# Performance work log

Hardware: AMD Instinct MI355X
Metric: run time of the kernel (lower is better)

## Reference

```python
import jax, jax.numpy as jnp
import numpy as np

EPS = 1e-06

def feature_map(x):
    # ELU + 1 feature map (default in LinearAttention)
    return jax.nn.elu(x) + 1.0

def setup_inputs() -> dict:
    key = jax.random.key(0)
    kq, kk, kv = jax.random.split(key, 3)
    N, L, H, D = 4, 8192, 16, 64
    queries = jax.random.normal(kq, (N, L, H, D), dtype=jnp.float32)
    keys = jax.random.normal(kk, (N, L, H, D), dtype=jnp.float32)
    values = jax.random.normal(kv, (N, L, H, D), dtype=jnp.float32)
    return {"queries": queries, "keys": keys, "values": values}

def reference(queries, keys, values):
    # Q, K: [N, L, H, D] after ELU+1 feature map
    Q = feature_map(queries)
    K = feature_map(keys)
    # KV state: [N, H, D, M]
    KV = jnp.einsum('nshd,nshm->nhdm', K, values)
    # normalizer: Z[n,l,h] = 1 / (Q . sum_s K + eps)
    Z = 1.0 / (jnp.einsum('nlhd,nhd->nlh', Q, K.sum(axis=1)) + EPS)
    # NOTE: faithful to original: KV (nhdm) is labeled 'nhmd' in the einsum,
    # i.e. KV is used transposed on its last two axes (requires D == M).
    V = jnp.einsum('nlhd,nhmd,nlh->nlhm', Q, KV, Z)
    return V
```

## Files before the change

kernel.cpp:

```cpp
#include <hip/hip_runtime.h>
#include <hip/hip_bf16.h>

#define LDIM 8192
#define HDIM 16
#define DDIM 64
#define NHEADPAIR 64
#define ROWSTRIDE 1024
#define KVSZ 4160
#define EPSF 1e-6f
#define CHUNKS 128
#define RPB 64
#define LROW 36

typedef float f32x4 __attribute__((ext_vector_type(4)));
typedef short s16x8 __attribute__((ext_vector_type(8)));

__device__ __forceinline__ float featmap(float x) {
    return x > 0.0f ? x + 1.0f : __expf(x);
}

__device__ __forceinline__ unsigned int pack_bf16x2(float a, float b) {
    union { __hip_bfloat162 h; unsigned int u; } x;
    x.h = __float22bfloat162_rn(make_float2(a, b));
    return x.u;
}

__device__ __forceinline__ unsigned short bf16_of(float a) {
    union { __hip_bfloat16 h; unsigned short u; } cv;
    cv.h = __float2bfloat16(a);
    return cv.u;
}

__device__ __forceinline__ int swz(int d) { return ((d >> 3) & 3) << 2; }

__global__ __launch_bounds__(256) void kv_oneshot_kernel(
    const float* __restrict__ Kp, const float* __restrict__ Vp,
    unsigned short* __restrict__ part)
{
    __shared__ unsigned int KT[64 * LROW];
    __shared__ unsigned int VT[64 * LROW];

    const int nh   = blockIdx.x;
    const int ch   = blockIdx.y;
    const int n    = nh >> 4;
    const int h    = nh & 15;
    const int t    = threadIdx.x;
    const int wave = t >> 6;
    const int lane = t & 63;

    const bool isK   = (t < 128);
    const int  uw    = (t >> 6) & 1;
    const int  col16 = lane & 15;
    const int  rv    = lane >> 4;
    const float* Sp  = isK ? Kp : Vp;
    const size_t base = (((size_t)n * LDIM + (size_t)ch * RPB) * HDIM + h) * DDIM
                      + col16 * 4;
    unsigned int* T = isK ? KT : VT;

#pragma unroll
    for (int g = 0; g < 4; ++g) {
        const int gg = uw * 4 + g;
        const int r1 = gg * 8 + rv;
        const int r2 = r1 + 4;
        float4 L1 = *(const float4*)(Sp + base + (size_t)r1 * ROWSTRIDE);
        float4 L2 = *(const float4*)(Sp + base + (size_t)r2 * ROWSTRIDE);
        float a[4] = { L1.x, L1.y, L1.z, L1.w };
        float b[4] = { L2.x, L2.y, L2.z, L2.w };
        if (isK) {
#pragma unroll
            for (int j = 0; j < 4; ++j) { a[j] = featmap(a[j]); b[j] = featmap(b[j]); }
        }
        const int slot = gg * 4 + rv;
#pragma unroll
        for (int j = 0; j < 4; ++j) {
            const int d = col16 * 4 + j;
            T[d * LROW + (slot ^ swz(d))] = pack_bf16x2(a[j], b[j]);
        }
    }
    __syncthreads();

    const int fr = lane & 15;
    const int fk = lane >> 4;
    const int d0 = wave * 16;

    f32x4 acc[4];
    f32x4 zac = (f32x4){0.f, 0.f, 0.f, 0.f};
#pragma unroll
    for (int mb = 0; mb < 4; ++mb) acc[mb] = (f32x4){0.f, 0.f, 0.f, 0.f};
    s16x8 ones;
#pragma unroll
    for (int i = 0; i < 8; ++i) ones[i] = (short)0x3F80;

    const int dA = d0 + fr;
#pragma unroll
    for (int kk = 0; kk < 2; ++kk) {
        const int slot = kk * 16 + fk * 4;
        s16x8 A = *(const s16x8*)&KT[dA * LROW + (slot ^ swz(dA))];
        zac = __builtin_amdgcn_mfma_f32_16x16x32_bf16(A, ones, zac, 0, 0, 0);
#pragma unroll
        for (int mb = 0; mb < 4; ++mb) {
            const int m = mb * 16 + fr;
            s16x8 B = *(const s16x8*)&VT[m * LROW + (slot ^ swz(m))];
            acc[mb] = __builtin_amdgcn_mfma_f32_16x16x32_bf16(A, B, acc[mb], 0, 0, 0);
        }
    }

    unsigned short* p = part + ((size_t)nh * CHUNKS + ch) * KVSZ;
#pragma unroll
    for (int mb = 0; mb < 4; ++mb)
#pragma unroll
        for (int reg = 0; reg < 4; ++reg)
            p[(d0 + fk * 4 + reg) * 64 + mb * 16 + fr] = bf16_of(acc[mb][reg]);
    if (fr == 0)
#pragma unroll
        for (int reg = 0; reg < 4; ++reg)
            p[4096 + d0 + fk * 4 + reg] = bf16_of(zac[reg]);
}

__global__ __launch_bounds__(256) void kv_reduce_kernel(
    const unsigned short* __restrict__ part, unsigned short* __restrict__ kvh)
{
    const int nh = blockIdx.y;
    const int e  = blockIdx.x * 256 + threadIdx.x;
    if (e >= KVSZ) return;
    float s = 0.0f;
    for (int c = 0; c < CHUNKS; ++c) {
        union { unsigned short u; __hip_bfloat16 h; } cv;
        cv.u = part[((size_t)nh * CHUNKS + c) * KVSZ + e];
        s += __bfloat162float(cv.h);
    }
    kvh[(size_t)nh * KVSZ + e] = bf16_of(s);
}

__global__ __launch_bounds__(256) void attn_mfma_kernel(
    const float* __restrict__ Qp, const unsigned short* __restrict__ kvh,
    float* __restrict__ out)
{
    __shared__ unsigned int kvU[64][36];
    __shared__ unsigned int ksU[36];
    __shared__ unsigned int qU[128][36];

    const int nh = blockIdx.y;
    const int n  = nh >> 4;
    const int h  = nh & 15;
    const int t  = threadIdx.x;

    {
        const unsigned int* kvg = (const unsigned int*)(kvh + (size_t)nh * KVSZ);
        const int r  = t >> 2;
        const int c0 = (t & 3) * 8;
        uint4 x = *(const uint4*)(kvg + r * 32 + c0);
        uint4 y = *(const uint4*)(kvg + r * 32 + c0 + 4);
        *(uint4*)&kvU[r][c0]     = x;
        *(uint4*)&kvU[r][c0 + 4] = y;
        if (t < 32) ksU[t] = kvg[2048 + t];
    }

    {
        const int qr = t >> 1;
        const float* qg = Qp + ((((size_t)n * LDIM) + (size_t)blockIdx.x * 128 + qr)
                                * HDIM + h) * DDIM + (t & 1) * 32;
        unsigned int q[16];
#pragma unroll
        for (int j = 0; j < 8; ++j) {
            float4 f = *(const float4*)(qg + j * 4);
            q[2 * j]     = pack_bf16x2(featmap(f.x), featmap(f.y));
            q[2 * j + 1] = pack_bf16x2(featmap(f.z), featmap(f.w));
        }
        uint4* dst = (uint4*)&qU[qr][(t & 1) * 16];
        dst[0] = make_uint4(q[0],  q[1],  q[2],  q[3]);
        dst[1] = make_uint4(q[4],  q[5],  q[6],  q[7]);
        dst[2] = make_uint4(q[8],  q[9],  q[10], q[11]);
        dst[3] = make_uint4(q[12], q[13], q[14], q[15]);
    }
    __syncthreads();

    const int wave = t >> 6;
    const int lane = t & 63;
    const int fr = lane & 15;
    const int fk = lane >> 4;

    s16x8 bF[4][2], kF[2];
#pragma unroll
    for (int mt = 0; mt < 4; ++mt)
#pragma unroll
        for (int kk = 0; kk < 2; ++kk)
            bF[mt][kk] = *(const s16x8*)&kvU[mt * 16 + fr][kk * 16 + fk * 4];
#pragma unroll
    for (int kk = 0; kk < 2; ++kk)
        kF[kk] = *(const s16x8*)&ksU[kk * 16 + fk * 4];

    f32x4 acc[2][4];
    f32x4 zac[2];
#pragma unroll
    for (int lt = 0; lt < 2; ++lt) {
        zac[lt] = (f32x4){0.f, 0.f, 0.f, 0.f};
#pragma unroll
        for (int mt = 0; mt < 4; ++mt) acc[lt][mt] = (f32x4){0.f, 0.f, 0.f, 0.f};
    }

#pragma unroll
    for (int kk = 0; kk < 2; ++kk) {
#pragma unroll
        for (int lt = 0; lt < 2; ++lt) {
            s16x8 A = *(const s16x8*)&qU[wave * 32 + lt * 16 + fr][kk * 16 + fk * 4];
            zac[lt] = __builtin_amdgcn_mfma_f32_16x16x32_bf16(A, kF[kk], zac[lt], 0, 0, 0);
#pragma unroll
            for (int mt = 0; mt < 4; ++mt)
                acc[lt][mt] = __builtin_amdgcn_mfma_f32_16x16x32_bf16(
                    A, bF[mt][kk], acc[lt][mt], 0, 0, 0);
        }
    }

#pragma unroll
    for (int lt = 0; lt < 2; ++lt) {
#pragma unroll
        for (int reg = 0; reg < 4; ++reg) {
            const int row = blockIdx.x * 128 + wave * 32 + lt * 16 + fk * 4 + reg;
            const float z = 1.0f / (zac[lt][reg] + EPSF);
            float* orow = out + (((size_t)n * LDIM + row) * HDIM + h) * DDIM;
#pragma unroll
            for (int mt = 0; mt < 4; ++mt)
                orow[mt * 16 + fr] = acc[lt][mt][reg] * z;
        }
    }
}

extern "C" void kernel_launch(void* const* d_in, const int* in_sizes, int n_in,
                              void* d_out, int out_size, void* d_ws, size_t ws_size,
                              hipStream_t stream) {
    const float* Q = (const float*)d_in[0];
    const float* K = (const float*)d_in[1];
    const float* V = (const float*)d_in[2];
    float* out = (float*)d_out;

    unsigned short* part = (unsigned short*)d_ws;
    unsigned short* kvh  = part + (size_t)NHEADPAIR * CHUNKS * KVSZ;

    dim3 g1(NHEADPAIR, CHUNKS);
    kv_oneshot_kernel<<<g1, 256, 0, stream>>>(K, V, part);
    dim3 gr((KVSZ + 255) / 256, NHEADPAIR);
    kv_reduce_kernel<<<gr, 256, 0, stream>>>(part, kvh);
    dim3 g2(LDIM / 128, NHEADPAIR);
    attn_mfma_kernel<<<g2, 256, 0, stream>>>(Q, kvh, out);
}
```

Measured before the change: 156.3 us.

## Restructure KV partial kernel to load 8 heads per block with dense rows

The KV partial kernel now has each 512-thread block cover 8 heads (half the heads of a batch) and 128 rows, looped in four 32-row tiles. Each row segment it loads is then a contiguous 512-byte span across heads, so global reads coalesce better. Halving the chunk count also halves the partial writes and the work of the reduce kernel. The costs are fewer blocks in the grid (8x64), a barrier pair per tile, and padded LDS strides that replace the XOR swizzle.

```diff
diff --git a/kernel.cpp b/kernel.cpp
--- a/kernel.cpp
+++ b/kernel.cpp
@@ -8,9 +8,12 @@
 #define ROWSTRIDE 1024
 #define KVSZ 4160
 #define EPSF 1e-6f
-#define CHUNKS 128
-#define RPB 64
-#define LROW 36
+#define CHUNKS 64
+#define RPB 128
+#define TROWS 32
+#define NT 4
+#define DSTR 17
+#define HSTR (64 * DSTR + 5)
 
 typedef float f32x4 __attribute__((ext_vector_type(4)));
 typedef short s16x8 __attribute__((ext_vector_type(8)));
@@ -31,90 +34,114 @@
     return cv.u;
 }
 
-__device__ __forceinline__ int swz(int d) { return ((d >> 3) & 3) << 2; }
-
-__global__ __launch_bounds__(256) void kv_oneshot_kernel(
+__global__ __launch_bounds__(512) void kv_dense_kernel(
     const float* __restrict__ Kp, const float* __restrict__ Vp,
     unsigned short* __restrict__ part)
 {
-    __shared__ unsigned int KT[64 * LROW];
-    __shared__ unsigned int VT[64 * LROW];
-
-    const int nh   = blockIdx.x;
+    __shared__ unsigned int KT[8 * HSTR];
+    __shared__ unsigned int VT[8 * HSTR];
+
+    const int nhf  = blockIdx.x;
+    const int n    = nhf >> 1;
+    const int half = nhf & 1;
     const int ch   = blockIdx.y;
-    const int n    = nh >> 4;
-    const int h    = nh & 15;
     const int t    = threadIdx.x;
     const int wave = t >> 6;
     const int lane = t & 63;
 
-    const bool isK   = (t < 128);
-    const int  uw    = (t >> 6) & 1;
-    const int  col16 = lane & 15;
-    const int  rv    = lane >> 4;
-    const float* Sp  = isK ? Kp : Vp;
-    const size_t base = (((size_t)n * LDIM + (size_t)ch * RPB) * HDIM + h) * DDIM
-                      + col16 * 4;
-    unsigned int* T = isK ? KT : VT;
-
-#pragma unroll
-    for (int g = 0; g < 4; ++g) {
-        const int gg = uw * 4 + g;
-        const int r1 = gg * 8 + rv;
-        const int r2 = r1 + 4;
-        float4 L1 = *(const float4*)(Sp + base + (size_t)r1 * ROWSTRIDE);
-        float4 L2 = *(const float4*)(Sp + base + (size_t)r2 * ROWSTRIDE);
-        float a[4] = { L1.x, L1.y, L1.z, L1.w };
-        float b[4] = { L2.x, L2.y, L2.z, L2.w };
-        if (isK) {
-#pragma unroll
-            for (int j = 0; j < 4; ++j) { a[j] = featmap(a[j]); b[j] = featmap(b[j]); }
-        }
-        const int slot = gg * 4 + rv;
-#pragma unroll
-        for (int j = 0; j < 4; ++j) {
-            const int d = col16 * 4 + j;
-            T[d * LROW + (slot ^ swz(d))] = pack_bf16x2(a[j], b[j]);
-        }
-    }
-    __syncthreads();
+    const int rb    = t >> 7;
+    const int pos   = t & 127;
+    const int headl = pos >> 4;
+    const int dq    = pos & 15;
+
+    const float4* K4 = (const float4*)Kp;
+    const float4* V4 = (const float4*)Vp;
 
     const int fr = lane & 15;
     const int fk = lane >> 4;
-    const int d0 = wave * 16;
-
-    f32x4 acc[4];
-    f32x4 zac = (f32x4){0.f, 0.f, 0.f, 0.f};
-#pragma unroll
-    for (int mb = 0; mb < 4; ++mb) acc[mb] = (f32x4){0.f, 0.f, 0.f, 0.f};
+
+    f32x4 acc[4][4];
+    f32x4 zac[4];
+#pragma unroll
+    for (int b = 0; b < 4; ++b) {
+        zac[b] = (f32x4){0.f, 0.f, 0.f, 0.f};
+#pragma unroll
+        for (int mb = 0; mb < 4; ++mb) acc[b][mb] = (f32x4){0.f, 0.f, 0.f, 0.f};
+    }
     s16x8 ones;
 #pragma unroll
     for (int i = 0; i < 8; ++i) ones[i] = (short)0x3F80;
 
-    const int dA = d0 + fr;
-#pragma unroll
-    for (int kk = 0; kk < 2; ++kk) {
-        const int slot = kk * 16 + fk * 4;
-        s16x8 A = *(const s16x8*)&KT[dA * LROW + (slot ^ swz(dA))];
-        zac = __builtin_amdgcn_mfma_f32_16x16x32_bf16(A, ones, zac, 0, 0, 0);
+    unsigned int* KTh = &KT[headl * HSTR];
+    unsigned int* VTh = &VT[headl * HSTR];
+    const unsigned int* KTw = &KT[wave * HSTR];
+    const unsigned int* VTw = &VT[wave * HSTR];
+
+    for (int tt = 0; tt < NT; ++tt) {
+        const size_t rowbase = (size_t)n * LDIM + (size_t)ch * RPB + tt * TROWS;
+
+#pragma unroll
+        for (int pb = 0; pb < 4; ++pb) {
+            const int rlo = rb + 8 * pb;
+            const int rhi = rlo + 4;
+            const size_t gl = (rowbase + rlo) * 256 + half * 128 + headl * 16 + dq;
+            const size_t gh = (rowbase + rhi) * 256 + half * 128 + headl * 16 + dq;
+            float4 kl = K4[gl];
+            float4 kh = K4[gh];
+            float4 vl = V4[gl];
+            float4 vh = V4[gh];
+            float klf[4] = { featmap(kl.x), featmap(kl.y), featmap(kl.z), featmap(kl.w) };
+            float khf[4] = { featmap(kh.x), featmap(kh.y), featmap(kh.z), featmap(kh.w) };
+            float vlf[4] = { vl.x, vl.y, vl.z, vl.w };
+            float vhf[4] = { vh.x, vh.y, vh.z, vh.w };
+            const int s = rb + 4 * pb;
+#pragma unroll
+            for (int j = 0; j < 4; ++j) {
+                const int d = dq * 4 + j;
+                KTh[d * DSTR + s] = pack_bf16x2(klf[j], khf[j]);
+                VTh[d * DSTR + s] = pack_bf16x2(vlf[j], vhf[j]);
+            }
+        }
+        __syncthreads();
+
+        union frag { unsigned int u[4]; s16x8 v; };
+        frag Bf[4];
 #pragma unroll
         for (int mb = 0; mb < 4; ++mb) {
-            const int m = mb * 16 + fr;
-            s16x8 B = *(const s16x8*)&VT[m * LROW + (slot ^ swz(m))];
-            acc[mb] = __builtin_amdgcn_mfma_f32_16x16x32_bf16(A, B, acc[mb], 0, 0, 0);
-        }
-    }
-
+            const int m = 16 * mb + fr;
+#pragma unroll
+            for (int c = 0; c < 4; ++c) Bf[mb].u[c] = VTw[m * DSTR + fk * 4 + c];
+        }
+#pragma unroll
+        for (int b = 0; b < 4; ++b) {
+            frag Af;
+            const int d = 16 * b + fr;
+#pragma unroll
+            for (int c = 0; c < 4; ++c) Af.u[c] = KTw[d * DSTR + fk * 4 + c];
+            zac[b] = __builtin_amdgcn_mfma_f32_16x16x32_bf16(Af.v, ones, zac[b], 0, 0, 0);
+#pragma unroll
+            for (int mb = 0; mb < 4; ++mb)
+                acc[b][mb] = __builtin_amdgcn_mfma_f32_16x16x32_bf16(
+                    Af.v, Bf[mb].v, acc[b][mb], 0, 0, 0);
+        }
+        __syncthreads();
+    }
+
+    const int nh = n * 16 + half * 8 + wave;
     unsigned short* p = part + ((size_t)nh * CHUNKS + ch) * KVSZ;
 #pragma unroll
-    for (int mb = 0; mb < 4; ++mb)
-#pragma unroll
-        for (int reg = 0; reg < 4; ++reg)
-            p[(d0 + fk * 4 + reg) * 64 + mb * 16 + fr] = bf16_of(acc[mb][reg]);
+    for (int b = 0; b < 4; ++b)
+#pragma unroll
+        for (int mb = 0; mb < 4; ++mb)
+#pragma unroll
+            for (int reg = 0; reg < 4; ++reg)
+                p[(16 * b + 4 * fk + reg) * 64 + 16 * mb + fr] = bf16_of(acc[b][mb][reg]);
     if (fr == 0)
 #pragma unroll
-        for (int reg = 0; reg < 4; ++reg)
-            p[4096 + d0 + fk * 4 + reg] = bf16_of(zac[reg]);
+        for (int b = 0; b < 4; ++b)
+#pragma unroll
+            for (int reg = 0; reg < 4; ++reg)
+                p[4096 + 16 * b + 4 * fk + reg] = bf16_of(zac[b][reg]);
 }
 
 __global__ __launch_bounds__(256) void kv_reduce_kernel(
@@ -237,8 +264,8 @@
     unsigned short* part = (unsigned short*)d_ws;
     unsigned short* kvh  = part + (size_t)NHEADPAIR * CHUNKS * KVSZ;
 
-    dim3 g1(NHEADPAIR, CHUNKS);
-    kv_oneshot_kernel<<<g1, 256, 0, stream>>>(K, V, part);
+    dim3 g1(8, CHUNKS);
+    kv_dense_kernel<<<g1, 512, 0, stream>>>(K, V, part);
     dim3 gr((KVSZ + 255) / 256, NHEADPAIR);
     kv_reduce_kernel<<<gr, 256, 0, stream>>>(part, kvh);
     dim3 g2(LDIM / 128, NHEADPAIR);
```

Result: faster. 147.2 us (-5.8%).
